# Optimization experiments

Hardware: AMD Instinct MI355X
Metric: run time of the kernel (lower is better)

Reference implementation:

```python
import jax, jax.numpy as jnp
import numpy as np

EPS = 1e-12  # matches torch F.normalize eps


def _l2_normalize(x):
    # F.normalize(x, p=2, dim=1): divide by clamped norm
    norm = jnp.sqrt(jnp.sum(x * x, axis=1, keepdims=True))
    return x / jnp.maximum(norm, EPS)


def setup_inputs() -> dict:
    key = jax.random.key(0)
    k1, k2, k3 = jax.random.split(key, 3)
    N, D, P, C = 16384, 768, 2048, 1000
    h = jax.random.normal(k1, (N, D), dtype=jnp.float32)
    prototypes = jax.random.normal(k2, (P, D), dtype=jnp.float32) * 0.1
    prototype_class = jax.random.normal(k3, (P, C), dtype=jnp.float32)
    temperature = jnp.float32(1.0)
    return {"h": h, "prototypes": prototypes,
            "prototype_class": prototype_class, "temperature": temperature}


def reference(h, prototypes, prototype_class, temperature):
    h_norm = _l2_normalize(h)                      # [N, D]
    p_norm = _l2_normalize(prototypes)             # [P, D]
    # cdist (p=2): sqrt(||a||^2 + ||b||^2 - 2 a.b), clamped at 0
    h_sq = jnp.sum(h_norm * h_norm, axis=1, keepdims=True)   # [N, 1]
    p_sq = jnp.sum(p_norm * p_norm, axis=1)                  # [P]
    dots = jnp.einsum('nd,pd->np', h_norm, p_norm)           # [N, P]
    dist_sq = jnp.maximum(h_sq + p_sq[None, :] - 2.0 * dots, 0.0)
    distances = jnp.sqrt(dist_sq)                            # [N, P]
    tau = jax.nn.softplus(temperature)
    activations = jnp.exp(-tau * distances)                  # [N, P]
    class_logits = jnp.matmul(activations, prototype_class)  # [N, C]
    return class_logits
```

## Files before the change

kernel.cpp:

```cpp
#include <hip/hip_runtime.h>
#include <hip/hip_bf16.h>
#include <math.h>

typedef unsigned short ushort_t;
typedef unsigned char uchar_t;
typedef unsigned int uint_t;
typedef __attribute__((ext_vector_type(8))) short bf16x8;
typedef __attribute__((ext_vector_type(4))) float f32x4;

#define AS1 __attribute__((address_space(1)))
#define AS3 __attribute__((address_space(3)))

__device__ __forceinline__ void gld_lds16(const void* g, void* l) {
  __builtin_amdgcn_global_load_lds((const AS1 void*)g, (AS3 void*)l, 16, 0, 0);
}

__device__ __forceinline__ ushort_t f32_to_bf16_bits(float v) {
  __hip_bfloat16 b = __float2bfloat16(v);
  return *(ushort_t*)&b;
}

__device__ __forceinline__ uint_t pack_fp8x4(float4 v, float sc) {
  int r = __builtin_amdgcn_cvt_pk_fp8_f32(v.x * sc, v.y * sc, 0, false);
  r = __builtin_amdgcn_cvt_pk_fp8_f32(v.z * sc, v.w * sc, r, true);
  return (uint_t)r;
}


__global__ __launch_bounds__(256) void prep(const float4* __restrict__ h,
                                            uchar_t* __restrict__ h8, int rowsH,
                                            const float4* __restrict__ p,
                                            uchar_t* __restrict__ p8, int rowsP,
                                            const float* __restrict__ pc,
                                            ushort_t* __restrict__ pcT,
                                            int P, int C, int normBlocks) {
  __shared__ float tile[32][33];
  if ((int)blockIdx.x < normBlocks) {
    int r = (blockIdx.x * 256 + threadIdx.x) >> 6;
    const int lane = threadIdx.x & 63;
    const float4* xr;
    uchar_t* o8;
    if (r < rowsH) {
      xr = h + (size_t)r * 192;
      o8 = h8;
    } else {
      r -= rowsH;
      if (r >= rowsP) return;
      xr = p + (size_t)r * 192;
      o8 = p8;
    }
    float4 v0 = xr[lane];
    float4 v1 = xr[lane + 64];
    float4 v2 = xr[lane + 128];
    float ss = v0.x * v0.x + v0.y * v0.y + v0.z * v0.z + v0.w * v0.w
             + v1.x * v1.x + v1.y * v1.y + v1.z * v1.z + v1.w * v1.w
             + v2.x * v2.x + v2.y * v2.y + v2.z * v2.z + v2.w * v2.w;
#pragma unroll
    for (int off = 32; off > 0; off >>= 1) ss += __shfl_xor(ss, off, 64);
    const float sc = 4.0f / fmaxf(sqrtf(ss), 1e-12f);
    const int rb = r >> 4, rl = r & 15;
    const int key = (rl >> 1) & 7;
    const int cc = (lane & 15) >> 1;
    const int cphys = ((cc ^ key) << 3) + ((lane & 1) << 2);
    const int ktb = lane >> 4;
    uchar_t* rowbase = o8 + (size_t)rb * 12 * 1024 + rl * 64 + cphys;
    *(uint_t*)(rowbase + (size_t)(ktb) * 1024)     = pack_fp8x4(v0, sc);
    *(uint_t*)(rowbase + (size_t)(4 + ktb) * 1024) = pack_fp8x4(v1, sc);
    *(uint_t*)(rowbase + (size_t)(8 + ktb) * 1024) = pack_fp8x4(v2, sc);
  } else {
    const int b = blockIdx.x - normBlocks;
    const int nkb = P / 32;
    const int bk = b % nkb, bc = b / nkb;
    const int k0 = bk * 32, c0 = bc * 32;
    const int tx = threadIdx.x & 31, ty = threadIdx.x >> 5;
#pragma unroll
    for (int rr = 0; rr < 4; ++rr) {
      const int c = c0 + tx;
      tile[ty + rr * 8][tx] = (c < C) ? pc[(size_t)(k0 + ty + rr * 8) * C + c] : 0.f;
    }
    __syncthreads();
    const int c2 = tx >> 3, off = tx & 7;
#pragma unroll
    for (int rr = 0; rr < 4; ++rr) {
      const int row = c0 + ty + rr * 8;
      const int rb = row >> 4, rl = row & 15;
      const int key4 = (rl >> 1) & 3;
      size_t us = (((size_t)rb * nkb + bk) * 16 + rl) * 32 + ((c2 ^ key4) << 3) + off;
      pcT[us] = f32_to_bf16_bits(tile[tx][ty + rr * 8]);
    }
  }
}

__launch_bounds__(256)
__global__ void gemm1_fp8(const uchar_t* __restrict__ A, const uchar_t* __restrict__ B,
                          ushort_t* __restrict__ act, const float* __restrict__ tptr,
                          int nKt, int actKT, int gx, int gxlog2) {
  __shared__ __align__(16) uchar_t As[16384];
  __shared__ __align__(16) uchar_t Bs[16384];
  const int tid = threadIdx.x, lane = tid & 63, wave = tid >> 6;
  const int wm = wave >> 1, wn = wave & 1;
  const int lid = blockIdx.x, xcd = lid & 7, q = lid >> 3;
  const int t = q & (gx - 1);
  const int s = ((q >> gxlog2) << 3) | xcd;

  f32x4 acc[4][4];
#pragma unroll
  for (int i = 0; i < 4; ++i)
#pragma unroll
    for (int j = 0; j < 4; ++j) acc[i][j] = (f32x4){0.f, 0.f, 0.f, 0.f};

  const uchar_t* aW = A + ((size_t)(s * 8 + 2 * wave) * nKt) * 1024 + lane * 16;
  const uchar_t* bW = B + ((size_t)(t * 8 + 2 * wave) * nKt) * 1024 + lane * 16;
  const size_t rstride = (size_t)nKt * 1024;
  uchar_t* lA = &As[wave * 4096];
  uchar_t* lB = &Bs[wave * 4096];

  const int fr = lane & 15, g = lane >> 4;
  const int key = (fr >> 1) & 7;
  const int rowoff = fr * 64;
  const int cp0 = ((g ^ key) << 3);
  const int cp1 = (((g | 4) ^ key) << 3);

  const int nIter = nKt >> 1;
  for (int kt = 0; kt < nIter; ++kt) {
    const size_t koff = (size_t)(2 * kt) * 1024;
    __syncthreads();
    gld_lds16(aW + koff, lA);
    gld_lds16(aW + koff + 1024, lA + 1024);
    gld_lds16(aW + rstride + koff, lA + 2048);
    gld_lds16(aW + rstride + koff + 1024, lA + 3072);
    gld_lds16(bW + koff, lB);
    gld_lds16(bW + koff + 1024, lB + 1024);
    gld_lds16(bW + rstride + koff, lB + 2048);
    gld_lds16(bW + rstride + koff + 1024, lB + 3072);
    __syncthreads();

#pragma unroll
    for (int kk = 0; kk < 2; ++kk) {
#pragma unroll
      for (int ksub = 0; ksub < 2; ++ksub) {
        const int cp = ksub ? cp1 : cp0;
        long a[4], b[4];
#pragma unroll
        for (int i = 0; i < 4; ++i)
          a[i] = *(const long*)&As[((wm * 4 + i) * 2 + kk) * 1024 + rowoff + cp];
#pragma unroll
        for (int j = 0; j < 4; ++j)
          b[j] = *(const long*)&Bs[((wn * 4 + j) * 2 + kk) * 1024 + rowoff + cp];
#pragma unroll
        for (int i = 0; i < 4; ++i)
#pragma unroll
          for (int j = 0; j < 4; ++j)
            acc[i][j] = __builtin_amdgcn_mfma_f32_16x16x32_fp8_fp8(a[i], b[j], acc[i][j], 0, 0, 0);
      }
    }
  }

  float tmp = *tptr;
  const float tau = log1pf(expf(tmp));
  const int crow = g * 4, ccol = fr;
  const int rowB = s * 128 + wm * 64, colB = t * 128 + wn * 64;
#pragma unroll
  for (int i = 0; i < 4; ++i)
#pragma unroll
    for (int j = 0; j < 4; ++j) {
      const int col = colB + j * 16 + ccol;
      const size_t ktile = col >> 5;
      const int c2 = (col >> 3) & 3, co = col & 7;
#pragma unroll
      for (int rr = 0; rr < 4; ++rr) {
        const int row = rowB + i * 16 + crow + rr;
        const int rb = row >> 4, rl = row & 15;
        const int key4 = (rl >> 1) & 3;
        float d2 = fmaxf(2.0f - acc[i][j][rr] * 0.125f, 0.0f);
        float d = d2 * rsqrtf(fmaxf(d2, 1e-20f));
        float a = __expf(-tau * d);
        act[(((size_t)rb * actKT + ktile) * 16 + rl) * 32 + ((c2 ^ key4) << 3) + co] =
            f32_to_bf16_bits(a);
      }
    }
}

#define BARRIER() do { asm volatile("" ::: "memory"); __builtin_amdgcn_s_barrier(); \
                       asm volatile("" ::: "memory"); } while (0)
#define LGKM0()   asm volatile("s_waitcnt lgkmcnt(0)" ::: "memory")
#define VM6()     asm volatile("s_waitcnt vmcnt(6)" ::: "memory")
#define VM0()     asm volatile("s_waitcnt vmcnt(0)" ::: "memory")
#define PRIO1()   __builtin_amdgcn_s_setprio(1)
#define PRIO0()   __builtin_amdgcn_s_setprio(0)
#define MM(a, b, c) __builtin_amdgcn_mfma_f32_16x16x32_bf16(a, b, c, 0, 0, 0)

#define MFMAQ(IB, AT, BL)                                          \
  acc[(IB) + 0][0] = MM(AT[0], BL[0], acc[(IB) + 0][0]);           \
  acc[(IB) + 1][0] = MM(AT[1], BL[0], acc[(IB) + 1][0]);           \
  acc[(IB) + 2][0] = MM(AT[2], BL[0], acc[(IB) + 2][0]);           \
  acc[(IB) + 3][0] = MM(AT[3], BL[0], acc[(IB) + 3][0]);           \
  acc[(IB) + 0][1] = MM(AT[0], BL[1], acc[(IB) + 0][1]);           \
  acc[(IB) + 1][1] = MM(AT[1], BL[1], acc[(IB) + 1][1]);           \
  acc[(IB) + 2][1] = MM(AT[2], BL[1], acc[(IB) + 2][1]);           \
  acc[(IB) + 3][1] = MM(AT[3], BL[1], acc[(IB) + 3][1]);           \
  acc[(IB) + 0][2] = MM(AT[0], BL[2], acc[(IB) + 0][2]);           \
  acc[(IB) + 1][2] = MM(AT[1], BL[2], acc[(IB) + 1][2]);           \
  acc[(IB) + 2][2] = MM(AT[2], BL[2], acc[(IB) + 2][2]);           \
  acc[(IB) + 3][2] = MM(AT[3], BL[2], acc[(IB) + 3][2]);           \
  acc[(IB) + 0][3] = MM(AT[0], BL[3], acc[(IB) + 0][3]);           \
  acc[(IB) + 1][3] = MM(AT[1], BL[3], acc[(IB) + 1][3]);           \
  acc[(IB) + 2][3] = MM(AT[2], BL[3], acc[(IB) + 2][3]);           \
  acc[(IB) + 3][3] = MM(AT[3], BL[3], acc[(IB) + 3][3])

__launch_bounds__(512, 2)
__global__ void gemm2_bf16_bal(const ushort_t* __restrict__ A,
                               const ushort_t* __restrict__ B,
                               float* __restrict__ out, int ldc, int ncols,
                               int nKt) {
  __shared__ __align__(16) uchar_t sm[131072];
  const int tid = threadIdx.x, lane = tid & 63, wave = tid >> 6;
  const int wm = wave >> 2, wn = wave & 3;
  const int lid = blockIdx.x, xcd = lid & 7, q = lid >> 3;
  const int tb = q & 3, sb = ((q >> 2) << 3) | xcd;

  f32x4 acc[8][4];
#pragma unroll
  for (int i = 0; i < 8; ++i)
#pragma unroll
    for (int j = 0; j < 4; ++j) acc[i][j] = (f32x4){0.f, 0.f, 0.f, 0.f};

  const int lw = wave & 1, rw = wave >> 1;
  const uchar_t* Apl = (const uchar_t*)A + ((size_t)(sb * 16) << 16) + (lw << 10) + lane * 16;
  const uchar_t* Bpl = (const uchar_t*)B + ((size_t)(tb * 16) << 16) + (lw << 10) + lane * 16;

  const int fr = lane & 15, g = lane >> 4;
  const int rdoff = fr * 64 + ((g ^ ((fr >> 1) & 3)) << 4);
  const int wm8 = wm * 8, wn4 = wn * 4;

#define STA(r_, T_, bo_) gld_lds16(Apl + (((size_t)(r_) << 16) + ((size_t)(T_) << 11)), \
                                   sm + (bo_) + ((((r_) << 1) + lw) << 10))
#define STB(r_, T_, bo_) gld_lds16(Bpl + (((size_t)(r_) << 16) + ((size_t)(T_) << 11)), \
                                   sm + (bo_) + 32768 + ((((r_) << 1) + lw) << 10))
#define DSA(i_, l_) (*(const bf16x8*)(sm + bufoff + (((wm8 + (i_)) * 2 + (l_)) << 10) + rdoff))
#define DSB(j_, l_) (*(const bf16x8*)(sm + bufoff + 32768 + (((wn4 + (j_)) * 2 + (l_)) << 10) + rdoff))

  STB(rw, 0, 0); STB(rw + 4, 0, 0); STB(rw + 8, 0, 0); STB(rw + 12, 0, 0);
  STA(rw, 0, 0); STA(rw + 8, 0, 0); STA(rw + 4, 0, 0); STA(rw + 12, 0, 0);
  STB(rw, 1, 65536); STB(rw + 4, 1, 65536); STB(rw + 8, 1, 65536); STB(rw + 12, 1, 65536);
  STA(rw, 1, 65536); STA(rw + 8, 1, 65536);
  VM6(); BARRIER();

  bf16x8 at[4], bl0[4], bl1[4];
  for (int kt = 0; kt < nKt; ++kt) {
    const int bufoff = (kt & 1) << 16;
    const int nbo = ((kt + 1) & 1) << 16;
    at[0] = DSA(0, 0); at[1] = DSA(1, 0); at[2] = DSA(2, 0); at[3] = DSA(3, 0);
    bl0[0] = DSB(0, 0); bl0[1] = DSB(1, 0); bl0[2] = DSB(2, 0); bl0[3] = DSB(3, 0);
    if (kt + 1 < nKt) { STA(rw + 4, kt + 1, nbo); STA(rw + 12, kt + 1, nbo); }
    BARRIER(); LGKM0();
    PRIO1(); MFMAQ(0, at, bl0); PRIO0();
    BARRIER();
    at[0] = DSA(4, 0); at[1] = DSA(5, 0); at[2] = DSA(6, 0); at[3] = DSA(7, 0);
    bl1[0] = DSB(0, 1); bl1[1] = DSB(1, 1); bl1[2] = DSB(2, 1); bl1[3] = DSB(3, 1);
    BARRIER(); LGKM0();
    PRIO1(); MFMAQ(4, at, bl0); PRIO0();
    BARRIER();
    at[0] = DSA(0, 1); at[1] = DSA(1, 1); at[2] = DSA(2, 1); at[3] = DSA(3, 1);
    if (kt + 2 < nKt) { STB(rw, kt + 2, bufoff); STB(rw + 4, kt + 2, bufoff); }
    BARRIER(); LGKM0();
    PRIO1(); MFMAQ(0, at, bl1); PRIO0();
    BARRIER();
    at[0] = DSA(4, 1); at[1] = DSA(5, 1); at[2] = DSA(6, 1); at[3] = DSA(7, 1);
    if (kt + 2 < nKt) {
      STB(rw + 8, kt + 2, bufoff); STB(rw + 12, kt + 2, bufoff);
      STA(rw, kt + 2, bufoff);     STA(rw + 8, kt + 2, bufoff);
    }
    BARRIER(); LGKM0();
    PRIO1(); MFMAQ(4, at, bl1); PRIO0();
    if (kt + 2 < nKt) { VM6(); } else { VM0(); }
    BARRIER();
  }

  const int crow = g * 4;
  const int rowB = sb * 256 + wm * 128, colB = tb * 256 + wn * 64;
#pragma unroll
  for (int i = 0; i < 8; ++i)
#pragma unroll
    for (int j = 0; j < 4; ++j) {
      const int col = colB + j * 16 + fr;
      if (col < ncols) {
#pragma unroll
        for (int rr = 0; rr < 4; ++rr)
          out[(size_t)(rowB + i * 16 + crow + rr) * ldc + col] = acc[i][j][rr];
      }
    }
}

extern "C" void kernel_launch(void* const* d_in, const int* in_sizes, int n_in,
                              void* d_out, int out_size, void* d_ws, size_t ws_size,
                              hipStream_t stream) {
  const float* h    = (const float*)d_in[0];
  const float* prot = (const float*)d_in[1];
  const float* pc   = (const float*)d_in[2];
  const float* temp = (const float*)d_in[3];
  float* out = (float*)d_out;

  const int D = 768;
  const int N = in_sizes[0] / D;
  const int P = in_sizes[1] / D;
  const int C = in_sizes[2] / P;
  const int CP = (C + 127) & ~127;

  char* ws = (char*)d_ws;
  size_t off = 0;
  uchar_t* h8   = (uchar_t*)(ws + off); off += (size_t)N * D;
  uchar_t* p8   = (uchar_t*)(ws + off); off += (size_t)P * D;
  ushort_t* pcT = (ushort_t*)(ws + off); off += (size_t)CP * P * 2;
  ushort_t* act = (ushort_t*)(ws + off); off += (size_t)N * P * 2;
  (void)ws_size;

  const int normBlocks = (N + P) / 4;
  const int transBlocks = (P / 32) * (CP / 32);
  prep<<<normBlocks + transBlocks, 256, 0, stream>>>(
      (const float4*)h, h8, N, (const float4*)prot, p8, P,
      pc, pcT, P, C, normBlocks);

  {
    const int GX = P / 128, GY = N / 128;
    gemm1_fp8<<<GX * GY, 256, 0, stream>>>(h8, p8, act, temp, D / 64, P / 32, GX, 4);
  }
  {
    const int GX = CP / 256, GY = N / 256;
    gemm2_bf16_bal<<<GX * GY, 512, 0, stream>>>(act, pcT, out, C, C, P / 64);
  }
}
```

Measured before the change: 224.2 us.

## Restructure second GEMM to 128x256 tiles with K=32 triple-buffered pipeline

Replaces the 256x256, K=64 double-buffered bf16 GEMM2 kernel with a 128x256 tile using a K-step of 32 and three rotating LDS buffers (72 KB instead of 128 KB). This doubles the number of blocks and shrinks per-thread accumulators, aiming at better occupancy, better load balance across CUs and simpler, less barrier-heavy scheduling. The trade-off is lower operand reuse per block, which means more global traffic for the B matrix, and shorter MFMA bursts between barriers.

```diff
diff --git a/kernel.cpp b/kernel.cpp
--- a/kernel.cpp
+++ b/kernel.cpp
@@ -184,103 +184,75 @@
 #define BARRIER() do { asm volatile("" ::: "memory"); __builtin_amdgcn_s_barrier(); \
                        asm volatile("" ::: "memory"); } while (0)
 #define LGKM0()   asm volatile("s_waitcnt lgkmcnt(0)" ::: "memory")
-#define VM6()     asm volatile("s_waitcnt vmcnt(6)" ::: "memory")
+#define VM3()     asm volatile("s_waitcnt vmcnt(3)" ::: "memory")
 #define VM0()     asm volatile("s_waitcnt vmcnt(0)" ::: "memory")
 #define PRIO1()   __builtin_amdgcn_s_setprio(1)
 #define PRIO0()   __builtin_amdgcn_s_setprio(0)
 #define MM(a, b, c) __builtin_amdgcn_mfma_f32_16x16x32_bf16(a, b, c, 0, 0, 0)
 
-#define MFMAQ(IB, AT, BL)                                          \
-  acc[(IB) + 0][0] = MM(AT[0], BL[0], acc[(IB) + 0][0]);           \
-  acc[(IB) + 1][0] = MM(AT[1], BL[0], acc[(IB) + 1][0]);           \
-  acc[(IB) + 2][0] = MM(AT[2], BL[0], acc[(IB) + 2][0]);           \
-  acc[(IB) + 3][0] = MM(AT[3], BL[0], acc[(IB) + 3][0]);           \
-  acc[(IB) + 0][1] = MM(AT[0], BL[1], acc[(IB) + 0][1]);           \
-  acc[(IB) + 1][1] = MM(AT[1], BL[1], acc[(IB) + 1][1]);           \
-  acc[(IB) + 2][1] = MM(AT[2], BL[1], acc[(IB) + 2][1]);           \
-  acc[(IB) + 3][1] = MM(AT[3], BL[1], acc[(IB) + 3][1]);           \
-  acc[(IB) + 0][2] = MM(AT[0], BL[2], acc[(IB) + 0][2]);           \
-  acc[(IB) + 1][2] = MM(AT[1], BL[2], acc[(IB) + 1][2]);           \
-  acc[(IB) + 2][2] = MM(AT[2], BL[2], acc[(IB) + 2][2]);           \
-  acc[(IB) + 3][2] = MM(AT[3], BL[2], acc[(IB) + 3][2]);           \
-  acc[(IB) + 0][3] = MM(AT[0], BL[3], acc[(IB) + 0][3]);           \
-  acc[(IB) + 1][3] = MM(AT[1], BL[3], acc[(IB) + 1][3]);           \
-  acc[(IB) + 2][3] = MM(AT[2], BL[3], acc[(IB) + 2][3]);           \
-  acc[(IB) + 3][3] = MM(AT[3], BL[3], acc[(IB) + 3][3])
-
-__launch_bounds__(512, 2)
-__global__ void gemm2_bf16_bal(const ushort_t* __restrict__ A,
-                               const ushort_t* __restrict__ B,
-                               float* __restrict__ out, int ldc, int ncols,
-                               int nKt) {
-  __shared__ __align__(16) uchar_t sm[131072];
+__launch_bounds__(512, 4)
+__global__ void gemm2_bf16_t3(const ushort_t* __restrict__ A,
+                              const ushort_t* __restrict__ B,
+                              float* __restrict__ out, int ldc, int ncols,
+                              int nKt) {
+  __shared__ __align__(16) uchar_t sm[73728];
   const int tid = threadIdx.x, lane = tid & 63, wave = tid >> 6;
   const int wm = wave >> 2, wn = wave & 3;
   const int lid = blockIdx.x, xcd = lid & 7, q = lid >> 3;
   const int tb = q & 3, sb = ((q >> 2) << 3) | xcd;
 
-  f32x4 acc[8][4];
-#pragma unroll
-  for (int i = 0; i < 8; ++i)
+  f32x4 acc[4][4];
+#pragma unroll
+  for (int i = 0; i < 4; ++i)
 #pragma unroll
     for (int j = 0; j < 4; ++j) acc[i][j] = (f32x4){0.f, 0.f, 0.f, 0.f};
 
-  const int lw = wave & 1, rw = wave >> 1;
-  const uchar_t* Apl = (const uchar_t*)A + ((size_t)(sb * 16) << 16) + (lw << 10) + lane * 16;
-  const uchar_t* Bpl = (const uchar_t*)B + ((size_t)(tb * 16) << 16) + (lw << 10) + lane * 16;
+  const uchar_t* Apl = (const uchar_t*)A + (((size_t)(sb * 8) * nKt) << 10) + lane * 16;
+  const uchar_t* Bpl = (const uchar_t*)B + (((size_t)(tb * 16) * nKt) << 10) + lane * 16;
 
   const int fr = lane & 15, g = lane >> 4;
   const int rdoff = fr * 64 + ((g ^ ((fr >> 1) & 3)) << 4);
-  const int wm8 = wm * 8, wn4 = wn * 4;
-
-#define STA(r_, T_, bo_) gld_lds16(Apl + (((size_t)(r_) << 16) + ((size_t)(T_) << 11)), \
-                                   sm + (bo_) + ((((r_) << 1) + lw) << 10))
-#define STB(r_, T_, bo_) gld_lds16(Bpl + (((size_t)(r_) << 16) + ((size_t)(T_) << 11)), \
-                                   sm + (bo_) + 32768 + ((((r_) << 1) + lw) << 10))
-#define DSA(i_, l_) (*(const bf16x8*)(sm + bufoff + (((wm8 + (i_)) * 2 + (l_)) << 10) + rdoff))
-#define DSB(j_, l_) (*(const bf16x8*)(sm + bufoff + 32768 + (((wn4 + (j_)) * 2 + (l_)) << 10) + rdoff))
-
-  STB(rw, 0, 0); STB(rw + 4, 0, 0); STB(rw + 8, 0, 0); STB(rw + 12, 0, 0);
-  STA(rw, 0, 0); STA(rw + 8, 0, 0); STA(rw + 4, 0, 0); STA(rw + 12, 0, 0);
-  STB(rw, 1, 65536); STB(rw + 4, 1, 65536); STB(rw + 8, 1, 65536); STB(rw + 12, 1, 65536);
-  STA(rw, 1, 65536); STA(rw + 8, 1, 65536);
-  VM6(); BARRIER();
-
-  bf16x8 at[4], bl0[4], bl1[4];
+  const uchar_t* smA = sm + (wm << 12) + rdoff;
+  const uchar_t* smB = sm + 8192 + (wn << 12) + rdoff;
+
+#define T3_STA(r_, T_, bo_) gld_lds16(Apl + ((size_t)((r_) * nKt + (T_)) << 10), \
+                                      sm + (bo_) + ((r_) << 10))
+#define T3_STB(c_, T_, bo_) gld_lds16(Bpl + ((size_t)((c_) * nKt + (T_)) << 10), \
+                                      sm + (bo_) + 8192 + ((c_) << 10))
+#define T3_DSA(bo_, i_) (*(const bf16x8*)(smA + (bo_) + ((i_) << 10)))
+#define T3_DSB(bo_, j_) (*(const bf16x8*)(smB + (bo_) + ((j_) << 10)))
+
+  T3_STA(wave, 0, 0); T3_STB(wave, 0, 0); T3_STB(wave + 8, 0, 0);
+  T3_STA(wave, 1, 24576); T3_STB(wave, 1, 24576); T3_STB(wave + 8, 1, 24576);
+  VM3(); BARRIER();
+
+  int boC = 0, boN = 24576, boNN = 49152;
   for (int kt = 0; kt < nKt; ++kt) {
-    const int bufoff = (kt & 1) << 16;
-    const int nbo = ((kt + 1) & 1) << 16;
-    at[0] = DSA(0, 0); at[1] = DSA(1, 0); at[2] = DSA(2, 0); at[3] = DSA(3, 0);
-    bl0[0] = DSB(0, 0); bl0[1] = DSB(1, 0); bl0[2] = DSB(2, 0); bl0[3] = DSB(3, 0);
-    if (kt + 1 < nKt) { STA(rw + 4, kt + 1, nbo); STA(rw + 12, kt + 1, nbo); }
+    bf16x8 a0 = T3_DSA(boC, 0), a1 = T3_DSA(boC, 1), a2 = T3_DSA(boC, 2), a3 = T3_DSA(boC, 3);
+    bf16x8 b0 = T3_DSB(boC, 0), b1 = T3_DSB(boC, 1), b2 = T3_DSB(boC, 2), b3 = T3_DSB(boC, 3);
+    if (kt + 2 < nKt) {
+      T3_STA(wave, kt + 2, boNN); T3_STB(wave, kt + 2, boNN); T3_STB(wave + 8, kt + 2, boNN);
+    }
     BARRIER(); LGKM0();
-    PRIO1(); MFMAQ(0, at, bl0); PRIO0();
+    PRIO1();
+    acc[0][0] = MM(a0, b0, acc[0][0]); acc[0][1] = MM(a0, b1, acc[0][1]);
+    acc[0][2] = MM(a0, b2, acc[0][2]); acc[0][3] = MM(a0, b3, acc[0][3]);
+    acc[1][0] = MM(a1, b0, acc[1][0]); acc[1][1] = MM(a1, b1, acc[1][1]);
+    acc[1][2] = MM(a1, b2, acc[1][2]); acc[1][3] = MM(a1, b3, acc[1][3]);
+    acc[2][0] = MM(a2, b0, acc[2][0]); acc[2][1] = MM(a2, b1, acc[2][1]);
+    acc[2][2] = MM(a2, b2, acc[2][2]); acc[2][3] = MM(a2, b3, acc[2][3]);
+    acc[3][0] = MM(a3, b0, acc[3][0]); acc[3][1] = MM(a3, b1, acc[3][1]);
+    acc[3][2] = MM(a3, b2, acc[3][2]); acc[3][3] = MM(a3, b3, acc[3][3]);
+    PRIO0();
+    if (kt + 2 < nKt) { VM3(); } else if (kt + 1 < nKt) { VM0(); }
     BARRIER();
-    at[0] = DSA(4, 0); at[1] = DSA(5, 0); at[2] = DSA(6, 0); at[3] = DSA(7, 0);
-    bl1[0] = DSB(0, 1); bl1[1] = DSB(1, 1); bl1[2] = DSB(2, 1); bl1[3] = DSB(3, 1);
-    BARRIER(); LGKM0();
-    PRIO1(); MFMAQ(4, at, bl0); PRIO0();
-    BARRIER();
-    at[0] = DSA(0, 1); at[1] = DSA(1, 1); at[2] = DSA(2, 1); at[3] = DSA(3, 1);
-    if (kt + 2 < nKt) { STB(rw, kt + 2, bufoff); STB(rw + 4, kt + 2, bufoff); }
-    BARRIER(); LGKM0();
-    PRIO1(); MFMAQ(0, at, bl1); PRIO0();
-    BARRIER();
-    at[0] = DSA(4, 1); at[1] = DSA(5, 1); at[2] = DSA(6, 1); at[3] = DSA(7, 1);
-    if (kt + 2 < nKt) {
-      STB(rw + 8, kt + 2, bufoff); STB(rw + 12, kt + 2, bufoff);
-      STA(rw, kt + 2, bufoff);     STA(rw + 8, kt + 2, bufoff);
-    }
-    BARRIER(); LGKM0();
-    PRIO1(); MFMAQ(4, at, bl1); PRIO0();
-    if (kt + 2 < nKt) { VM6(); } else { VM0(); }
-    BARRIER();
+    int tswap = boC; boC = boN; boN = boNN; boNN = tswap;
   }
 
   const int crow = g * 4;
-  const int rowB = sb * 256 + wm * 128, colB = tb * 256 + wn * 64;
-#pragma unroll
-  for (int i = 0; i < 8; ++i)
+  const int rowB = sb * 128 + wm * 64, colB = tb * 256 + wn * 64;
+#pragma unroll
+  for (int i = 0; i < 4; ++i)
 #pragma unroll
     for (int j = 0; j < 4; ++j) {
       const int col = colB + j * 16 + fr;
@@ -326,7 +298,7 @@
     gemm1_fp8<<<GX * GY, 256, 0, stream>>>(h8, p8, act, temp, D / 64, P / 32, GX, 4);
   }
   {
-    const int GX = CP / 256, GY = N / 256;
-    gemm2_bf16_bal<<<GX * GY, 512, 0, stream>>>(act, pcT, out, C, C, P / 64);
-  }
-}
+    const int GX = CP / 256, GY = N / 128;
+    gemm2_bf16_t3<<<GX * GY, 512, 0, stream>>>(act, pcT, out, C, C, P / 32);
+  }
+}
```

New measurement: 217.0 us. -3.2%, faster.
